# Performance work log

Hardware: AMD Instinct MI355X
Metric: run time of the kernel (lower is better)

Reference implementation:

```python
import jax, jax.numpy as jnp
import numpy as np
from jax import lax

B, N, C, HEADS, SR = 2, 4096, 256, 8, 2
HW = 64

def setup_inputs() -> dict:
    key = jax.random.key(0)
    ks = jax.random.split(key, 12)
    s = 0.02
    return {
        "x0": jax.random.normal(ks[0], (B, N, C), jnp.float32),
        "x1": jax.random.normal(ks[1], (B, N, C), jnp.float32),
        "Wq": jax.random.normal(ks[2], (C, C), jnp.float32) * s,
        "Wkv": jax.random.normal(ks[3], (2 * C, C), jnp.float32) * s,
        "Wproj": jax.random.normal(ks[4], (C, C), jnp.float32) * s,
        "bproj": jnp.zeros((C,), jnp.float32),
        "Wsr": jax.random.normal(ks[5], (C, C, SR, SR), jnp.float32) * np.sqrt(2.0 / (SR * SR * C)),
        "bsr": jnp.zeros((C,), jnp.float32),
        "ln_w0": jnp.ones((C,), jnp.float32),
        "ln_b0": jnp.zeros((C,), jnp.float32),
        "ln_w1": jnp.ones((C,), jnp.float32),
        "ln_b1": jnp.zeros((C,), jnp.float32),
        "H": HW,
        "W": HW,
    }

def _layernorm(x, w, b, eps=1e-5):
    mu = jnp.mean(x, axis=-1, keepdims=True)
    var = jnp.mean(jnp.square(x - mu), axis=-1, keepdims=True)
    return (x - mu) * lax.rsqrt(var + eps) * w + b

def _attend(x, ln_w, ln_b, Wq, Wkv, Wproj, bproj, Wsr, bsr, H, W):
    b, n, c = x.shape
    h = HEADS
    d = c // h
    scale = d ** -0.5
    # q: (B, h, N, d)
    q = (x @ Wq.T).reshape(b, n, h, d).transpose(0, 2, 1, 3)
    # spatial reduction: conv k=stride=sr on (B,C,H,W)
    xs = x.transpose(0, 2, 1).reshape(b, c, H, W)
    xs = lax.conv_general_dilated(xs, Wsr, (SR, SR), 'VALID',
                                  dimension_numbers=('NCHW', 'OIHW', 'NCHW'))
    xs = xs + bsr[None, :, None, None]
    m = (H // SR) * (W // SR)
    xs = xs.reshape(b, c, m).transpose(0, 2, 1)  # (B, M, C)
    xs = _layernorm(xs, ln_w, ln_b)
    kv = (xs @ Wkv.T).reshape(b, m, 2, h, d).transpose(2, 0, 3, 1, 4)
    k, v = kv[0], kv[1]  # (B, h, M, d)
    attn = jnp.einsum('bhnd,bhmd->bhnm', q, k) * scale
    attn = jax.nn.softmax(attn, axis=-1)
    out = jnp.einsum('bhnm,bhmd->bhnd', attn, v)
    out = out.transpose(0, 2, 1, 3).reshape(b, n, c)
    return out @ Wproj.T + bproj

def reference(x0, x1, Wq, Wkv, Wproj, bproj, Wsr, bsr, ln_w0, ln_b0, ln_w1, ln_b1, H, W):
    y0 = _attend(x0, ln_w0, ln_b0, Wq, Wkv, Wproj, bproj, Wsr, bsr, H, W)
    y1 = _attend(x1, ln_w1, ln_b1, Wq, Wkv, Wproj, bproj, Wsr, bsr, H, W)
    return (y0, y1)
```

## Files before the change

kernel.cpp:

```cpp
#include <hip/hip_runtime.h>
#include <hip/hip_bf16.h>
#include <cstddef>

typedef __hip_bfloat16 bf16;
typedef __attribute__((ext_vector_type(8))) short bf16x8;
typedef __attribute__((ext_vector_type(4))) float f32x4;
typedef __attribute__((ext_vector_type(4))) short short4v;

__device__ __forceinline__ float b2f(bf16 v) { return __bfloat162float(v); }
__device__ __forceinline__ bf16 f2b(float v) { return __float2bfloat16(v); }

#define MFMA(a, b, c) __builtin_amdgcn_mfma_f32_16x16x32_bf16((a), (b), (c), 0, 0, 0)

#define WQ_OFF   0
#define WKV_OFF  65536
#define WP_OFF   196608
#define WSR_OFF  262144

__global__ __launch_bounds__(256) void prep_cvt(
    const float* __restrict__ x0, const float* __restrict__ x1,
    bf16* __restrict__ xb,
    const float* __restrict__ Wq, const float* __restrict__ Wkv,
    const float* __restrict__ Wp, const float* __restrict__ Wsr,
    bf16* __restrict__ wb) {
  const int t = threadIdx.x;
  if (blockIdx.x < 1024) {
    const int gid = blockIdx.x * 256 + t;
    for (int i = gid; i < 1048576; i += 262144) {
      const float4 v = (i < 524288) ? ((const float4*)x0)[i]
                                    : ((const float4*)x1)[i - 524288];
      union { bf16 h[4]; short4v s; } u;
      u.h[0] = f2b(v.x); u.h[1] = f2b(v.y); u.h[2] = f2b(v.z); u.h[3] = f2b(v.w);
      ((short4v*)xb)[i] = u.s;
    }
  } else {
    const int gid = (blockIdx.x - 1024) * 256 + t;
    for (int i = gid; i < 524288; i += 131072) {
      float v;
      if (i < WKV_OFF)       v = Wq[i];
      else if (i < WP_OFF)   v = Wkv[i - WKV_OFF];
      else if (i < WSR_OFF)  v = Wp[i - WP_OFF];
      else {
        const int r = i - WSR_OFF;
        const int o = r >> 10, k = r & 1023;
        const int p = k >> 8, c = k & 255;
        v = Wsr[o * 1024 + c * 4 + p];
      }
      wb[i] = f2b(v);
    }
  }
}

#define STAGE_W(W_lds, wgl, ldg)                                             \
  _Pragma("unroll")                                                          \
  for (int u = 0; u < 8; ++u) {                                              \
    const int idx = u * 256 + t;                                             \
    const int wr = idx >> 5;                                                 \
    const int wc = (idx & 31) * 8;                                           \
    *(bf16x8*)&W_lds[wr][wc] = *(const bf16x8*)((wgl) + wr * (ldg) + wc);    \
  }

__global__ __launch_bounds__(256) void qc_mfma(
    const bf16* __restrict__ xb, const bf16* __restrict__ wb,
    const float* __restrict__ bsr, bf16* __restrict__ q,
    bf16* __restrict__ xsb) {
  __shared__ bf16 W_lds[64][264];
  const int t = threadIdx.x;
  const int wave = t >> 6, lane = t & 63, quad = lane >> 4, l16 = lane & 15;
  const int colh = blockIdx.y * 64;

  if (blockIdx.x < 256) {
    const int row0 = blockIdx.x * 64 + wave * 16;
    STAGE_W(W_lds, wb + WQ_OFF + colh * 256, 256);
    __syncthreads();
    const bf16* ap = xb + (row0 + l16) * 256 + quad * 8;
    f32x4 acc[4];
    #pragma unroll
    for (int j = 0; j < 4; ++j) acc[j] = (f32x4){0.f, 0.f, 0.f, 0.f};
    #pragma unroll
    for (int k0 = 0; k0 < 256; k0 += 32) {
      const bf16x8 af = *(const bf16x8*)(ap + k0);
      #pragma unroll
      for (int j = 0; j < 4; ++j) {
        const bf16x8 wf = *(const bf16x8*)&W_lds[j * 16 + l16][k0 + quad * 8];
        acc[j] = MFMA(af, wf, acc[j]);
      }
    }
    const float scale = 0.2550348572f;
    #pragma unroll
    for (int j = 0; j < 4; ++j)
      #pragma unroll
      for (int r = 0; r < 4; ++r)
        q[(row0 + quad * 4 + r) * 256 + colh + j * 16 + l16] =
            f2b(acc[j][r] * scale);
  } else {
    const int bx = blockIdx.x - 256;
    const int row0 = bx * 64 + wave * 16;
    const int mrow = row0 + l16;
    const int ab = mrow >> 10;
    const int m = mrow & 1023;
    const int mi_ = m >> 5, mj = m & 31;
    f32x4 acc[4];
    #pragma unroll
    for (int j = 0; j < 4; ++j) acc[j] = (f32x4){0.f, 0.f, 0.f, 0.f};
    for (int p = 0; p < 4; ++p) {
      __syncthreads();
      STAGE_W(W_lds, wb + WSR_OFF + colh * 1024 + p * 256, 1024);
      __syncthreads();
      const int n = (2 * mi_ + (p >> 1)) * 64 + 2 * mj + (p & 1);
      const bf16* ap = xb + (ab * 4096 + n) * 256 + quad * 8;
      #pragma unroll
      for (int c0 = 0; c0 < 256; c0 += 32) {
        const bf16x8 af = *(const bf16x8*)(ap + c0);
        #pragma unroll
        for (int j = 0; j < 4; ++j) {
          const bf16x8 wf = *(const bf16x8*)&W_lds[j * 16 + l16][c0 + quad * 8];
          acc[j] = MFMA(af, wf, acc[j]);
        }
      }
    }
    #pragma unroll
    for (int j = 0; j < 4; ++j) {
      const int col = colh + j * 16 + l16;
      const float bv = bsr[col];
      #pragma unroll
      for (int r = 0; r < 4; ++r)
        xsb[(row0 + quad * 4 + r) * 256 + col] = f2b(acc[j][r] + bv);
    }
  }
}

__global__ __launch_bounds__(256) void kvln_mfma(
    const bf16* __restrict__ xsb, const bf16* __restrict__ wb,
    const float* __restrict__ w0, const float* __restrict__ b0,
    const float* __restrict__ w1, const float* __restrict__ b1,
    bf16* __restrict__ kbuf, bf16* __restrict__ vbuf_t) {
  __shared__ bf16 W_lds[64][264];
  __shared__ float lnw[256], lnb[256];
  const int t = threadIdx.x;
  const int wave = t >> 6, lane = t & 63, quad = lane >> 4, l16 = lane & 15;
  const int row0 = blockIdx.x * 64 + wave * 16;
  const int colh = blockIdx.y * 64;
  const int a = (blockIdx.x * 64) >> 11;
  lnw[t] = a ? w1[t] : w0[t];
  lnb[t] = a ? b1[t] : b0[t];
  STAGE_W(W_lds, wb + WKV_OFF + colh * 256, 256);
  __syncthreads();

  const bf16* ap = xsb + (row0 + l16) * 256 + quad * 8;
  bf16x8 af[8];
  float sum = 0.f, ss = 0.f;
  #pragma unroll
  for (int i = 0; i < 8; ++i) {
    af[i] = *(const bf16x8*)(ap + i * 32);
    #pragma unroll
    for (int e = 0; e < 8; ++e) {
      const float x = b2f(((bf16*)&af[i])[e]);
      sum += x; ss += x * x;
    }
  }
  sum += __shfl_xor(sum, 16, 64); sum += __shfl_xor(sum, 32, 64);
  ss  += __shfl_xor(ss, 16, 64);  ss  += __shfl_xor(ss, 32, 64);
  const float mu = sum * (1.0f / 256.0f);
  const float var = ss * (1.0f / 256.0f) - mu * mu;
  const float rstd = rsqrtf(var + 1e-5f);
  #pragma unroll
  for (int i = 0; i < 8; ++i) {
    const int cb = i * 32 + quad * 8;
    union { bf16 h[8]; bf16x8 v; } u;
    #pragma unroll
    for (int e = 0; e < 8; ++e) {
      const float x = b2f(((bf16*)&af[i])[e]);
      u.h[e] = f2b((x - mu) * rstd * lnw[cb + e] + lnb[cb + e]);
    }
    af[i] = u.v;
  }

  f32x4 acc[4];
  #pragma unroll
  for (int j = 0; j < 4; ++j) acc[j] = (f32x4){0.f, 0.f, 0.f, 0.f};
  #pragma unroll
  for (int i = 0; i < 8; ++i) {
    #pragma unroll
    for (int j = 0; j < 4; ++j) {
      const bf16x8 wf = *(const bf16x8*)&W_lds[j * 16 + l16][i * 32 + quad * 8];
      acc[j] = MFMA(af[i], wf, acc[j]);
    }
  }
  #pragma unroll
  for (int j = 0; j < 4; ++j) {
    const int o = colh + j * 16 + l16;
    #pragma unroll
    for (int r = 0; r < 4; ++r) {
      const int row = row0 + quad * 4 + r;
      const int m = row & 1023;
      const bf16 val = f2b(acc[j][r]);
      if (o < 256) {
        const int h = o >> 5, d = o & 31;
        kbuf[((row >> 10) * 8 + h) * 32768 + m * 32 + d] = val;
      } else {
        const int o2 = o - 256;
        const int h = o2 >> 5, d = o2 & 31;
        const int rr = m & 63;
        const int mp = (m & ~63) | (rr & 32) | ((rr & 12) << 1) |
                       ((rr & 16) >> 2) | (rr & 3);
        vbuf_t[((row >> 10) * 8 + h) * 32768 + d * 1024 + mp] = val;
      }
    }
  }
}

__global__ __launch_bounds__(256) void attn_mfma(
    const bf16* __restrict__ q, const bf16* __restrict__ kbuf,
    const bf16* __restrict__ vbuf_t, bf16* __restrict__ att) {
  const int abh = blockIdx.y;
  const int ab = abh >> 3;
  const int h = abh & 7;
  const int t = threadIdx.x;
  const int lane = t & 63, quad = lane >> 4, l16 = lane & 15;
  const int qbase = blockIdx.x * 128 + (t >> 6) * 32;

  __shared__ bf16 KT[2][2048];
  __shared__ bf16 VT[2][2048];

  const bf16* kb = kbuf + abh * 32768;
  const bf16* vb = vbuf_t + abh * 32768;

  const int kg = (t >> 6) * 512 + ((t >> 2) & 15) * 32 + (t & 3) * 8;
  const int vg_row = (t >> 7) * 16 + ((t >> 3) & 15);
  const int vg_col = ((t >> 2) & 1) * 32 + (t & 3) * 8;

  bf16x8 qf[2];
  #pragma unroll
  for (int s = 0; s < 2; ++s)
    qf[s] = *(const bf16x8*)(
        q + (ab * 4096 + qbase + s * 16 + l16) * 256 + h * 32 + quad * 8);

  {
    const bf16x8 kr = *(const bf16x8*)(kb + kg);
    const bf16x8 vr = *(const bf16x8*)(vb + vg_row * 1024 + vg_col);
    *(bf16x8*)&KT[0][t * 8] = kr;
    *(bf16x8*)&VT[0][t * 8] = vr;
  }
  __syncthreads();

  f32x4 o[2][2];
  float lp[2] = {0.f, 0.f};
  #pragma unroll
  for (int s = 0; s < 2; ++s) {
    o[s][0] = (f32x4){0.f, 0.f, 0.f, 0.f};
    o[s][1] = (f32x4){0.f, 0.f, 0.f, 0.f};
  }
  const f32x4 zero = {0.f, 0.f, 0.f, 0.f};

  for (int kt = 0; kt < 16; ++kt) {
    const int cur = kt & 1;
    bf16x8 kr, vr;
    const bool pf = (kt + 1 < 16);
    if (pf) {
      const int nk0 = (kt + 1) * 64;
      kr = *(const bf16x8*)(kb + nk0 * 32 + kg);
      vr = *(const bf16x8*)(vb + vg_row * 1024 + nk0 + vg_col);
    }
    f32x4 S[2][4];
    #pragma unroll
    for (int tt = 0; tt < 4; ++tt) {
      const bf16x8 kf =
          *(const bf16x8*)&KT[cur][(tt * 64 + l16 * 4 + quad) * 8];
      S[0][tt] = MFMA(kf, qf[0], zero);
      S[1][tt] = MFMA(kf, qf[1], zero);
    }
    bf16x8 pa[2][2];
    #pragma unroll
    for (int s = 0; s < 2; ++s) {
      float p[4][4];
      float acc = 0.f;
      #pragma unroll
      for (int tt = 0; tt < 4; ++tt)
        #pragma unroll
        for (int r = 0; r < 4; ++r) {
          p[tt][r] = __builtin_amdgcn_exp2f(S[s][tt][r]);
          acc += p[tt][r];
        }
      lp[s] += acc;
      #pragma unroll
      for (int c2 = 0; c2 < 2; ++c2) {
        union { __hip_bfloat162 h2[4]; bf16x8 v; } u;
        u.h2[0] = __float22bfloat162_rn(float2{p[c2 * 2][0], p[c2 * 2][1]});
        u.h2[1] = __float22bfloat162_rn(float2{p[c2 * 2][2], p[c2 * 2][3]});
        u.h2[2] = __float22bfloat162_rn(float2{p[c2 * 2 + 1][0], p[c2 * 2 + 1][1]});
        u.h2[3] = __float22bfloat162_rn(float2{p[c2 * 2 + 1][2], p[c2 * 2 + 1][3]});
        pa[s][c2] = u.v;
      }
    }
    #pragma unroll
    for (int c2 = 0; c2 < 2; ++c2) {
      #pragma unroll
      for (int dh = 0; dh < 2; ++dh) {
        const bf16x8 vf = *(const bf16x8*)&VT[cur]
            [(dh * 128 + l16 * 8 + c2 * 4 + quad) * 8];
        o[0][dh] = MFMA(pa[0][c2], vf, o[0][dh]);
        o[1][dh] = MFMA(pa[1][c2], vf, o[1][dh]);
      }
    }
    if (pf) {
      *(bf16x8*)&KT[cur ^ 1][t * 8] = kr;
      *(bf16x8*)&VT[cur ^ 1][t * 8] = vr;
    }
    __syncthreads();
  }
  #pragma unroll
  for (int s = 0; s < 2; ++s) {
    lp[s] += __shfl_xor(lp[s], 16, 64);
    lp[s] += __shfl_xor(lp[s], 32, 64);
  }
  #pragma unroll
  for (int s = 0; s < 2; ++s) {
    #pragma unroll
    for (int r = 0; r < 4; ++r) {
      const float li = __shfl(lp[s], quad * 4 + r, 16);
      const float inv = 1.0f / li;
      const int qrow = ab * 4096 + qbase + s * 16 + quad * 4 + r;
      bf16* orow = att + qrow * 256 + h * 32;
      orow[l16]      = f2b(o[s][0][r] * inv);
      orow[16 + l16] = f2b(o[s][1][r] * inv);
    }
  }
}

__global__ __launch_bounds__(256) void proj_mfma(
    const bf16* __restrict__ att, const bf16* __restrict__ wb,
    const float* __restrict__ bp, float* __restrict__ outp) {
  __shared__ bf16 W_lds[64][264];
  const int t = threadIdx.x;
  const int wave = t >> 6, lane = t & 63, quad = lane >> 4, l16 = lane & 15;
  const int row0 = blockIdx.x * 64 + wave * 16;
  const int colh = blockIdx.y * 64;
  STAGE_W(W_lds, wb + WP_OFF + colh * 256, 256);
  __syncthreads();
  const bf16* ap = att + (row0 + l16) * 256 + quad * 8;
  f32x4 acc[4];
  #pragma unroll
  for (int j = 0; j < 4; ++j) acc[j] = (f32x4){0.f, 0.f, 0.f, 0.f};
  #pragma unroll
  for (int k0 = 0; k0 < 256; k0 += 32) {
    const bf16x8 af = *(const bf16x8*)(ap + k0);
    #pragma unroll
    for (int j = 0; j < 4; ++j) {
      const bf16x8 wf = *(const bf16x8*)&W_lds[j * 16 + l16][k0 + quad * 8];
      acc[j] = MFMA(af, wf, acc[j]);
    }
  }
  #pragma unroll
  for (int j = 0; j < 4; ++j) {
    const int col = colh + j * 16 + l16;
    const float bv = bp[col];
    #pragma unroll
    for (int r = 0; r < 4; ++r)
      outp[(row0 + quad * 4 + r) * 256 + col] = acc[j][r] + bv;
  }
}

extern "C" void kernel_launch(void* const* d_in, const int* in_sizes, int n_in,
                              void* d_out, int out_size, void* d_ws, size_t ws_size,
                              hipStream_t stream) {
  const float* x0    = (const float*)d_in[0];
  const float* x1    = (const float*)d_in[1];
  const float* Wq    = (const float*)d_in[2];
  const float* Wkv   = (const float*)d_in[3];
  const float* Wproj = (const float*)d_in[4];
  const float* bproj = (const float*)d_in[5];
  const float* Wsr   = (const float*)d_in[6];
  const float* bsr   = (const float*)d_in[7];
  const float* lnw0  = (const float*)d_in[8];
  const float* lnb0  = (const float*)d_in[9];
  const float* lnw1  = (const float*)d_in[10];
  const float* lnb1  = (const float*)d_in[11];

  bf16* q_bf   = (bf16*)d_out;
  bf16* xb     = q_bf + 4194304;
  bf16* att_bf = (bf16*)d_ws;
  bf16* xsb    = att_bf + 4194304;
  bf16* kbuf   = xsb + 1048576;
  bf16* vbuf_t = kbuf + 1048576;
  bf16* wb     = vbuf_t + 1048576;
  float* y     = (float*)d_out;

  const dim3 blk(256);
  prep_cvt<<<dim3(1536), blk, 0, stream>>>(x0, x1, xb, Wq, Wkv, Wproj, Wsr, wb);
  qc_mfma<<<dim3(320, 4), blk, 0, stream>>>(xb, wb, bsr, q_bf, xsb);
  kvln_mfma<<<dim3(64, 8), blk, 0, stream>>>(xsb, wb, lnw0, lnb0, lnw1, lnb1,
                                             kbuf, vbuf_t);
  attn_mfma<<<dim3(32, 32), blk, 0, stream>>>(q_bf, kbuf, vbuf_t, att_bf);
  proj_mfma<<<dim3(256, 4), blk, 0, stream>>>(att_bf, wb, bproj, y);
}
```

Baseline: 158.8 us.

## Fuse all stages into one cooperative persistent kernel with grid syncs

Replaces the five separate launches (convert, q/conv, kv+layernorm, attention, projection) with a single cooperative kernel of 512 persistent blocks that loop over work units and separate stages with grid-wide syncs. The aim is to remove per-launch overhead and inter-kernel gaps. The cost is that each stage now runs on a fixed 512-block grid with grid barriers and threadfences, which can reduce parallelism in some stages. The original multi-kernel path stays as a fallback if the cooperative launch fails.

```diff
diff --git a/kernel.cpp b/kernel.cpp
--- a/kernel.cpp
+++ b/kernel.cpp
@@ -1,6 +1,9 @@
 #include <hip/hip_runtime.h>
 #include <hip/hip_bf16.h>
+#include <hip/hip_cooperative_groups.h>
 #include <cstddef>
+
+namespace cg = cooperative_groups;
 
 typedef __hip_bfloat16 bf16;
 typedef __attribute__((ext_vector_type(8))) short bf16x8;
@@ -16,6 +19,16 @@
 #define WKV_OFF  65536
 #define WP_OFF   196608
 #define WSR_OFF  262144
+
+#define STAGE_W(W_lds, wgl, ldg)                                             \
+  _Pragma("unroll")                                                          \
+  for (int uu_ = 0; uu_ < 8; ++uu_) {                                        \
+    const int idx_ = uu_ * 256 + t;                                          \
+    const int wr_ = idx_ >> 5;                                               \
+    const int wc_ = (idx_ & 31) * 8;                                         \
+    *(bf16x8*)&W_lds[wr_][wc_] = *(const bf16x8*)((wgl) + wr_ * (ldg) + wc_);\
+  }
+
 
 __global__ __launch_bounds__(256) void prep_cvt(
     const float* __restrict__ x0, const float* __restrict__ x1,
@@ -50,15 +63,6 @@
     }
   }
 }
-
-#define STAGE_W(W_lds, wgl, ldg)                                             \
-  _Pragma("unroll")                                                          \
-  for (int u = 0; u < 8; ++u) {                                              \
-    const int idx = u * 256 + t;                                             \
-    const int wr = idx >> 5;                                                 \
-    const int wc = (idx & 31) * 8;                                           \
-    *(bf16x8*)&W_lds[wr][wc] = *(const bf16x8*)((wgl) + wr * (ldg) + wc);    \
-  }
 
 __global__ __launch_bounds__(256) void qc_mfma(
     const bf16* __restrict__ xb, const bf16* __restrict__ wb,
@@ -361,6 +365,342 @@
   }
 }
 
+__global__ __launch_bounds__(256, 2) void mega(
+    const float* x0, const float* x1,
+    const float* Wq, const float* Wkv,
+    const float* Wp, const float* Wsr,
+    const float* bsr, const float* bp,
+    const float* w0, const float* b0,
+    const float* w1, const float* b1,
+    bf16* xb, bf16* wb, bf16* q, bf16* xsb,
+    bf16* kbuf, bf16* vbuf_t, bf16* att, float* y) {
+  cg::grid_group grid = cg::this_grid();
+  __shared__ bf16 W_lds[64][264];
+  __shared__ bf16 KT[2][2048];
+  __shared__ bf16 VT[2][2048];
+  __shared__ float lnw[256], lnb[256];
+
+  const int t = threadIdx.x;
+  const int wave = t >> 6, lane = t & 63, quad = lane >> 4, l16 = lane & 15;
+  const int bid = blockIdx.x;
+  const int NB = gridDim.x;
+
+  {
+    const int gid = bid * 256 + t;
+    const int gs = NB * 256;
+    for (int i = gid; i < 1048576; i += gs) {
+      const float4 v = (i < 524288) ? ((const float4*)x0)[i]
+                                    : ((const float4*)x1)[i - 524288];
+      union { bf16 h[4]; short4v s; } u;
+      u.h[0] = f2b(v.x); u.h[1] = f2b(v.y); u.h[2] = f2b(v.z); u.h[3] = f2b(v.w);
+      ((short4v*)xb)[i] = u.s;
+    }
+    for (int i = gid; i < 524288; i += gs) {
+      float v;
+      if (i < WKV_OFF)       v = Wq[i];
+      else if (i < WP_OFF)   v = Wkv[i - WKV_OFF];
+      else if (i < WSR_OFF)  v = Wp[i - WP_OFF];
+      else {
+        const int r = i - WSR_OFF;
+        const int o = r >> 10, k = r & 1023;
+        const int p = k >> 8, c = k & 255;
+        v = Wsr[o * 1024 + c * 4 + p];
+      }
+      wb[i] = f2b(v);
+    }
+  }
+  __threadfence(); grid.sync(); __threadfence();
+
+  for (int u = bid; u < 512; u += NB) {
+    if (u < 256) {
+      const int cx = u & 63, cy = u >> 6;
+      const int row0 = cx * 64 + wave * 16;
+      const int colh = cy * 64;
+      const int mrow = row0 + l16;
+      const int ab = mrow >> 10;
+      const int m = mrow & 1023;
+      const int mi_ = m >> 5, mj = m & 31;
+      f32x4 acc[4];
+      #pragma unroll
+      for (int j = 0; j < 4; ++j) acc[j] = (f32x4){0.f, 0.f, 0.f, 0.f};
+      for (int p = 0; p < 4; ++p) {
+        __syncthreads();
+        STAGE_W(W_lds, wb + WSR_OFF + colh * 1024 + p * 256, 1024);
+        __syncthreads();
+        const int n = (2 * mi_ + (p >> 1)) * 64 + 2 * mj + (p & 1);
+        const bf16* ap = xb + (ab * 4096 + n) * 256 + quad * 8;
+        #pragma unroll
+        for (int c0 = 0; c0 < 256; c0 += 32) {
+          const bf16x8 af = *(const bf16x8*)(ap + c0);
+          #pragma unroll
+          for (int j = 0; j < 4; ++j) {
+            const bf16x8 wf = *(const bf16x8*)&W_lds[j * 16 + l16][c0 + quad * 8];
+            acc[j] = MFMA(af, wf, acc[j]);
+          }
+        }
+      }
+      #pragma unroll
+      for (int j = 0; j < 4; ++j) {
+        const int col = colh + j * 16 + l16;
+        const float bv = bsr[col];
+        #pragma unroll
+        for (int r = 0; r < 4; ++r)
+          xsb[(row0 + quad * 4 + r) * 256 + col] = f2b(acc[j][r] + bv);
+      }
+    } else {
+      const int idx = u - 256;
+      const int colh = (idx >> 6) * 64;
+      __syncthreads();
+      STAGE_W(W_lds, wb + WQ_OFF + colh * 256, 256);
+      __syncthreads();
+      const float scale = 0.2550348572f;
+      for (int ii = 0; ii < 4; ++ii) {
+        const int row0 = ((idx & 63) * 4 + ii) * 64 + wave * 16;
+        const bf16* ap = xb + (row0 + l16) * 256 + quad * 8;
+        f32x4 acc[4];
+        #pragma unroll
+        for (int j = 0; j < 4; ++j) acc[j] = (f32x4){0.f, 0.f, 0.f, 0.f};
+        #pragma unroll
+        for (int k0 = 0; k0 < 256; k0 += 32) {
+          const bf16x8 af = *(const bf16x8*)(ap + k0);
+          #pragma unroll
+          for (int j = 0; j < 4; ++j) {
+            const bf16x8 wf = *(const bf16x8*)&W_lds[j * 16 + l16][k0 + quad * 8];
+            acc[j] = MFMA(af, wf, acc[j]);
+          }
+        }
+        #pragma unroll
+        for (int j = 0; j < 4; ++j)
+          #pragma unroll
+          for (int r = 0; r < 4; ++r)
+            q[(row0 + quad * 4 + r) * 256 + colh + j * 16 + l16] =
+                f2b(acc[j][r] * scale);
+      }
+    }
+  }
+  __threadfence(); grid.sync(); __threadfence();
+
+  for (int u = bid; u < 512; u += NB) {
+    const int kx = u & 63;
+    const int colh = (u >> 6) * 64;
+    const int row0 = kx * 64 + wave * 16;
+    const int a = (kx * 64) >> 11;
+    __syncthreads();
+    lnw[t] = a ? w1[t] : w0[t];
+    lnb[t] = a ? b1[t] : b0[t];
+    STAGE_W(W_lds, wb + WKV_OFF + colh * 256, 256);
+    __syncthreads();
+
+    const bf16* ap = xsb + (row0 + l16) * 256 + quad * 8;
+    bf16x8 af[8];
+    float sum = 0.f, ss = 0.f;
+    #pragma unroll
+    for (int i = 0; i < 8; ++i) {
+      af[i] = *(const bf16x8*)(ap + i * 32);
+      #pragma unroll
+      for (int e = 0; e < 8; ++e) {
+        const float x = b2f(((bf16*)&af[i])[e]);
+        sum += x; ss += x * x;
+      }
+    }
+    sum += __shfl_xor(sum, 16, 64); sum += __shfl_xor(sum, 32, 64);
+    ss  += __shfl_xor(ss, 16, 64);  ss  += __shfl_xor(ss, 32, 64);
+    const float mu = sum * (1.0f / 256.0f);
+    const float var = ss * (1.0f / 256.0f) - mu * mu;
+    const float rstd = rsqrtf(var + 1e-5f);
+    #pragma unroll
+    for (int i = 0; i < 8; ++i) {
+      const int cb = i * 32 + quad * 8;
+      union { bf16 h[8]; bf16x8 v; } uu;
+      #pragma unroll
+      for (int e = 0; e < 8; ++e) {
+        const float x = b2f(((bf16*)&af[i])[e]);
+        uu.h[e] = f2b((x - mu) * rstd * lnw[cb + e] + lnb[cb + e]);
+      }
+      af[i] = uu.v;
+    }
+
+    f32x4 acc[4];
+    #pragma unroll
+    for (int j = 0; j < 4; ++j) acc[j] = (f32x4){0.f, 0.f, 0.f, 0.f};
+    #pragma unroll
+    for (int i = 0; i < 8; ++i) {
+      #pragma unroll
+      for (int j = 0; j < 4; ++j) {
+        const bf16x8 wf = *(const bf16x8*)&W_lds[j * 16 + l16][i * 32 + quad * 8];
+        acc[j] = MFMA(af[i], wf, acc[j]);
+      }
+    }
+    #pragma unroll
+    for (int j = 0; j < 4; ++j) {
+      const int o = colh + j * 16 + l16;
+      #pragma unroll
+      for (int r = 0; r < 4; ++r) {
+        const int row = row0 + quad * 4 + r;
+        const int m = row & 1023;
+        const bf16 val = f2b(acc[j][r]);
+        if (o < 256) {
+          const int h = o >> 5, d = o & 31;
+          kbuf[((row >> 10) * 8 + h) * 32768 + m * 32 + d] = val;
+        } else {
+          const int o2 = o - 256;
+          const int h = o2 >> 5, d = o2 & 31;
+          const int rr = m & 63;
+          const int mp = (m & ~63) | (rr & 32) | ((rr & 12) << 1) |
+                         ((rr & 16) >> 2) | (rr & 3);
+          vbuf_t[((row >> 10) * 8 + h) * 32768 + d * 1024 + mp] = val;
+        }
+      }
+    }
+  }
+  __threadfence(); grid.sync(); __threadfence();
+
+  {
+    const int kg = (t >> 6) * 512 + ((t >> 2) & 15) * 32 + (t & 3) * 8;
+    const int vg_row = (t >> 7) * 16 + ((t >> 3) & 15);
+    const int vg_col = ((t >> 2) & 1) * 32 + (t & 3) * 8;
+    const f32x4 zero = {0.f, 0.f, 0.f, 0.f};
+
+    for (int unit = bid; unit < 1024; unit += NB) {
+      const int abh = unit >> 5;
+      const int ab = abh >> 3;
+      const int h = abh & 7;
+      const int qbase = (unit & 31) * 128 + wave * 32;
+
+      const bf16* kb = kbuf + abh * 32768;
+      const bf16* vb = vbuf_t + abh * 32768;
+
+      bf16x8 qf[2];
+      #pragma unroll
+      for (int s = 0; s < 2; ++s)
+        qf[s] = *(const bf16x8*)(
+            q + (ab * 4096 + qbase + s * 16 + l16) * 256 + h * 32 + quad * 8);
+
+      {
+        const bf16x8 kr = *(const bf16x8*)(kb + kg);
+        const bf16x8 vr = *(const bf16x8*)(vb + vg_row * 1024 + vg_col);
+        *(bf16x8*)&KT[0][t * 8] = kr;
+        *(bf16x8*)&VT[0][t * 8] = vr;
+      }
+      __syncthreads();
+
+      f32x4 o[2][2];
+      float lp[2] = {0.f, 0.f};
+      #pragma unroll
+      for (int s = 0; s < 2; ++s) {
+        o[s][0] = (f32x4){0.f, 0.f, 0.f, 0.f};
+        o[s][1] = (f32x4){0.f, 0.f, 0.f, 0.f};
+      }
+
+      for (int kt = 0; kt < 16; ++kt) {
+        const int cur = kt & 1;
+        bf16x8 kr, vr;
+        const bool pfl = (kt + 1 < 16);
+        if (pfl) {
+          const int nk0 = (kt + 1) * 64;
+          kr = *(const bf16x8*)(kb + nk0 * 32 + kg);
+          vr = *(const bf16x8*)(vb + vg_row * 1024 + nk0 + vg_col);
+        }
+        f32x4 S[2][4];
+        #pragma unroll
+        for (int tt = 0; tt < 4; ++tt) {
+          const bf16x8 kf =
+              *(const bf16x8*)&KT[cur][(tt * 64 + l16 * 4 + quad) * 8];
+          S[0][tt] = MFMA(kf, qf[0], zero);
+          S[1][tt] = MFMA(kf, qf[1], zero);
+        }
+        bf16x8 pa[2][2];
+        #pragma unroll
+        for (int s = 0; s < 2; ++s) {
+          float p[4][4];
+          float acc = 0.f;
+          #pragma unroll
+          for (int tt = 0; tt < 4; ++tt)
+            #pragma unroll
+            for (int r = 0; r < 4; ++r) {
+              p[tt][r] = __builtin_amdgcn_exp2f(S[s][tt][r]);
+              acc += p[tt][r];
+            }
+          lp[s] += acc;
+          #pragma unroll
+          for (int c2 = 0; c2 < 2; ++c2) {
+            union { __hip_bfloat162 h2[4]; bf16x8 v; } uu;
+            uu.h2[0] = __float22bfloat162_rn(float2{p[c2 * 2][0], p[c2 * 2][1]});
+            uu.h2[1] = __float22bfloat162_rn(float2{p[c2 * 2][2], p[c2 * 2][3]});
+            uu.h2[2] = __float22bfloat162_rn(float2{p[c2 * 2 + 1][0], p[c2 * 2 + 1][1]});
+            uu.h2[3] = __float22bfloat162_rn(float2{p[c2 * 2 + 1][2], p[c2 * 2 + 1][3]});
+            pa[s][c2] = uu.v;
+          }
+        }
+        #pragma unroll
+        for (int c2 = 0; c2 < 2; ++c2) {
+          #pragma unroll
+          for (int dh = 0; dh < 2; ++dh) {
+            const bf16x8 vf = *(const bf16x8*)&VT[cur]
+                [(dh * 128 + l16 * 8 + c2 * 4 + quad) * 8];
+            o[0][dh] = MFMA(pa[0][c2], vf, o[0][dh]);
+            o[1][dh] = MFMA(pa[1][c2], vf, o[1][dh]);
+          }
+        }
+        if (pfl) {
+          *(bf16x8*)&KT[cur ^ 1][t * 8] = kr;
+          *(bf16x8*)&VT[cur ^ 1][t * 8] = vr;
+        }
+        __syncthreads();
+      }
+      #pragma unroll
+      for (int s = 0; s < 2; ++s) {
+        lp[s] += __shfl_xor(lp[s], 16, 64);
+        lp[s] += __shfl_xor(lp[s], 32, 64);
+      }
+      #pragma unroll
+      for (int s = 0; s < 2; ++s) {
+        #pragma unroll
+        for (int r = 0; r < 4; ++r) {
+          const float li = __shfl(lp[s], quad * 4 + r, 16);
+          const float inv = 1.0f / li;
+          const int qrow = ab * 4096 + qbase + s * 16 + quad * 4 + r;
+          bf16* orow = att + qrow * 256 + h * 32;
+          orow[l16]      = f2b(o[s][0][r] * inv);
+          orow[16 + l16] = f2b(o[s][1][r] * inv);
+        }
+      }
+    }
+  }
+  __threadfence(); grid.sync(); __threadfence();
+
+  for (int u = bid; u < 512; u += NB) {
+    const int colh = (u >> 7) * 64;
+    __syncthreads();
+    STAGE_W(W_lds, wb + WP_OFF + colh * 256, 256);
+    __syncthreads();
+    for (int ii = 0; ii < 2; ++ii) {
+      const int row0 = ((u & 127) * 2 + ii) * 64 + wave * 16;
+      const bf16* ap = att + (row0 + l16) * 256 + quad * 8;
+      f32x4 acc[4];
+      #pragma unroll
+      for (int j = 0; j < 4; ++j) acc[j] = (f32x4){0.f, 0.f, 0.f, 0.f};
+      #pragma unroll
+      for (int k0 = 0; k0 < 256; k0 += 32) {
+        const bf16x8 af = *(const bf16x8*)(ap + k0);
+        #pragma unroll
+        for (int j = 0; j < 4; ++j) {
+          const bf16x8 wf = *(const bf16x8*)&W_lds[j * 16 + l16][k0 + quad * 8];
+          acc[j] = MFMA(af, wf, acc[j]);
+        }
+      }
+      #pragma unroll
+      for (int j = 0; j < 4; ++j) {
+        const int col = colh + j * 16 + l16;
+        const float bv = bp[col];
+        #pragma unroll
+        for (int r = 0; r < 4; ++r)
+          y[(row0 + quad * 4 + r) * 256 + col] = acc[j][r] + bv;
+      }
+    }
+  }
+}
+
 extern "C" void kernel_launch(void* const* d_in, const int* in_sizes, int n_in,
                               void* d_out, int out_size, void* d_ws, size_t ws_size,
                               hipStream_t stream) {
@@ -386,11 +726,37 @@
   bf16* wb     = vbuf_t + 1048576;
   float* y     = (float*)d_out;
 
-  const dim3 blk(256);
-  prep_cvt<<<dim3(1536), blk, 0, stream>>>(x0, x1, xb, Wq, Wkv, Wproj, Wsr, wb);
-  qc_mfma<<<dim3(320, 4), blk, 0, stream>>>(xb, wb, bsr, q_bf, xsb);
-  kvln_mfma<<<dim3(64, 8), blk, 0, stream>>>(xsb, wb, lnw0, lnb0, lnw1, lnb1,
-                                             kbuf, vbuf_t);
-  attn_mfma<<<dim3(32, 32), blk, 0, stream>>>(q_bf, kbuf, vbuf_t, att_bf);
-  proj_mfma<<<dim3(256, 4), blk, 0, stream>>>(att_bf, wb, bproj, y);
+  static int coop_ok = -1;
+  if (coop_ok < 0) {
+    int maxB = 0;
+    hipError_t e =
+        hipOccupancyMaxActiveBlocksPerMultiprocessor(&maxB, mega, 256, 0);
+    coop_ok = (e == hipSuccess && maxB >= 2) ? 1 : 0;
+  }
+
+  bool launched = false;
+  if (coop_ok == 1) {
+    void* args[] = {
+        (void*)&x0, (void*)&x1, (void*)&Wq, (void*)&Wkv, (void*)&Wproj,
+        (void*)&Wsr, (void*)&bsr, (void*)&bproj, (void*)&lnw0, (void*)&lnb0,
+        (void*)&lnw1, (void*)&lnb1, (void*)&xb, (void*)&wb, (void*)&q_bf,
+        (void*)&xsb, (void*)&kbuf, (void*)&vbuf_t, (void*)&att_bf, (void*)&y};
+    hipError_t e = hipLaunchCooperativeKernel(mega, dim3(512), dim3(256),
+                                              args, 0u, stream);
+    if (e == hipSuccess) {
+      launched = true;
+    } else {
+      coop_ok = 0;
+    }
+  }
+
+  if (!launched) {
+    const dim3 blk(256);
+    prep_cvt<<<dim3(1536), blk, 0, stream>>>(x0, x1, xb, Wq, Wkv, Wproj, Wsr, wb);
+    qc_mfma<<<dim3(320, 4), blk, 0, stream>>>(xb, wb, bsr, q_bf, xsb);
+    kvln_mfma<<<dim3(64, 8), blk, 0, stream>>>(xsb, wb, lnw0, lnb0, lnw1, lnb1,
+                                               kbuf, vbuf_t);
+    attn_mfma<<<dim3(32, 32), blk, 0, stream>>>(q_bf, kbuf, vbuf_t, att_bf);
+    proj_mfma<<<dim3(256, 4), blk, 0, stream>>>(att_bf, wb, bproj, y);
+  }
 }
```

Measured after the change: 160.7 us. No clear change (+1.2%).

## Fuse fp32-to-bf16 conversion into GEMM kernels and swizzle V tile in LDS

Applied to the files above, without the earlier changes.

Removes the separate prep_cvt kernel and converts x and all weight matrices from fp32 to bf16 on the fly inside the Q/conv, KV and projection kernels. This saves one launch and a full round trip of the converted activations through global memory. The cost is that each GEMM now reads fp32 data, twice the bytes per element, and x is re-read by each of the 4 column blocks. The conv weight gather is also strided. Separately, the V tile in LDS is XOR-swizzled on write and read to reduce bank conflicts in the attention PV MFMA loads.

```diff
diff --git a/kernel.cpp b/kernel.cpp
--- a/kernel.cpp
+++ b/kernel.cpp
@@ -12,56 +12,49 @@
 
 #define MFMA(a, b, c) __builtin_amdgcn_mfma_f32_16x16x32_bf16((a), (b), (c), 0, 0, 0)
 
-#define WQ_OFF   0
-#define WKV_OFF  65536
-#define WP_OFF   196608
-#define WSR_OFF  262144
-
-__global__ __launch_bounds__(256) void prep_cvt(
+__device__ __forceinline__ bf16x8 cvt8f(const float* p) {
+  const float4 a = *(const float4*)p;
+  const float4 b = *(const float4*)(p + 4);
+  union { __hip_bfloat162 h2[4]; bf16x8 v; } u;
+  u.h2[0] = __float22bfloat162_rn(float2{a.x, a.y});
+  u.h2[1] = __float22bfloat162_rn(float2{a.z, a.w});
+  u.h2[2] = __float22bfloat162_rn(float2{b.x, b.y});
+  u.h2[3] = __float22bfloat162_rn(float2{b.z, b.w});
+  return u.v;
+}
+
+__device__ __forceinline__ const float* xrow_ptr(
+    const float* x0, const float* x1, int rr) {
+  return (rr < 8192) ? (x0 + rr * 256) : (x1 + (rr - 8192) * 256);
+}
+
+#define STAGE_WF(W_lds, wgl, ldg)                                            \
+  _Pragma("unroll")                                                          \
+  for (int uu_ = 0; uu_ < 8; ++uu_) {                                        \
+    const int idx_ = uu_ * 256 + t;                                          \
+    const int wr_ = idx_ >> 5;                                               \
+    const int wc_ = (idx_ & 31) * 8;                                         \
+    *(bf16x8*)&W_lds[wr_][wc_] = cvt8f((wgl) + wr_ * (ldg) + wc_);           \
+  }
+
+#define STAGE_WSR(W_lds, Wsr, colh, p)                                       \
+  _Pragma("unroll")                                                          \
+  for (int uu_ = 0; uu_ < 8; ++uu_) {                                        \
+    const int idx_ = uu_ * 256 + t;                                          \
+    const int wr_ = idx_ >> 5;                                               \
+    const int wc_ = (idx_ & 31) * 8;                                         \
+    const float* wp_ = (Wsr) + ((colh) + wr_) * 1024 + wc_ * 4 + (p);        \
+    union { __hip_bfloat162 h2[4]; bf16x8 v; } u_;                           \
+    u_.h2[0] = __float22bfloat162_rn(float2{wp_[0],  wp_[4]});               \
+    u_.h2[1] = __float22bfloat162_rn(float2{wp_[8],  wp_[12]});              \
+    u_.h2[2] = __float22bfloat162_rn(float2{wp_[16], wp_[20]});              \
+    u_.h2[3] = __float22bfloat162_rn(float2{wp_[24], wp_[28]});              \
+    *(bf16x8*)&W_lds[wr_][wc_] = u_.v;                                       \
+  }
+
+__global__ __launch_bounds__(256) void qc_mfma(
     const float* __restrict__ x0, const float* __restrict__ x1,
-    bf16* __restrict__ xb,
-    const float* __restrict__ Wq, const float* __restrict__ Wkv,
-    const float* __restrict__ Wp, const float* __restrict__ Wsr,
-    bf16* __restrict__ wb) {
-  const int t = threadIdx.x;
-  if (blockIdx.x < 1024) {
-    const int gid = blockIdx.x * 256 + t;
-    for (int i = gid; i < 1048576; i += 262144) {
-      const float4 v = (i < 524288) ? ((const float4*)x0)[i]
-                                    : ((const float4*)x1)[i - 524288];
-      union { bf16 h[4]; short4v s; } u;
-      u.h[0] = f2b(v.x); u.h[1] = f2b(v.y); u.h[2] = f2b(v.z); u.h[3] = f2b(v.w);
-      ((short4v*)xb)[i] = u.s;
-    }
-  } else {
-    const int gid = (blockIdx.x - 1024) * 256 + t;
-    for (int i = gid; i < 524288; i += 131072) {
-      float v;
-      if (i < WKV_OFF)       v = Wq[i];
-      else if (i < WP_OFF)   v = Wkv[i - WKV_OFF];
-      else if (i < WSR_OFF)  v = Wp[i - WP_OFF];
-      else {
-        const int r = i - WSR_OFF;
-        const int o = r >> 10, k = r & 1023;
-        const int p = k >> 8, c = k & 255;
-        v = Wsr[o * 1024 + c * 4 + p];
-      }
-      wb[i] = f2b(v);
-    }
-  }
-}
-
-#define STAGE_W(W_lds, wgl, ldg)                                             \
-  _Pragma("unroll")                                                          \
-  for (int u = 0; u < 8; ++u) {                                              \
-    const int idx = u * 256 + t;                                             \
-    const int wr = idx >> 5;                                                 \
-    const int wc = (idx & 31) * 8;                                           \
-    *(bf16x8*)&W_lds[wr][wc] = *(const bf16x8*)((wgl) + wr * (ldg) + wc);    \
-  }
-
-__global__ __launch_bounds__(256) void qc_mfma(
-    const bf16* __restrict__ xb, const bf16* __restrict__ wb,
+    const float* __restrict__ Wq, const float* __restrict__ Wsr,
     const float* __restrict__ bsr, bf16* __restrict__ q,
     bf16* __restrict__ xsb) {
   __shared__ bf16 W_lds[64][264];
@@ -71,15 +64,15 @@
 
   if (blockIdx.x < 256) {
     const int row0 = blockIdx.x * 64 + wave * 16;
-    STAGE_W(W_lds, wb + WQ_OFF + colh * 256, 256);
+    STAGE_WF(W_lds, Wq + colh * 256, 256);
     __syncthreads();
-    const bf16* ap = xb + (row0 + l16) * 256 + quad * 8;
+    const float* ap = xrow_ptr(x0, x1, row0 + l16) + quad * 8;
     f32x4 acc[4];
     #pragma unroll
     for (int j = 0; j < 4; ++j) acc[j] = (f32x4){0.f, 0.f, 0.f, 0.f};
     #pragma unroll
     for (int k0 = 0; k0 < 256; k0 += 32) {
-      const bf16x8 af = *(const bf16x8*)(ap + k0);
+      const bf16x8 af = cvt8f(ap + k0);
       #pragma unroll
       for (int j = 0; j < 4; ++j) {
         const bf16x8 wf = *(const bf16x8*)&W_lds[j * 16 + l16][k0 + quad * 8];
@@ -105,13 +98,13 @@
     for (int j = 0; j < 4; ++j) acc[j] = (f32x4){0.f, 0.f, 0.f, 0.f};
     for (int p = 0; p < 4; ++p) {
       __syncthreads();
-      STAGE_W(W_lds, wb + WSR_OFF + colh * 1024 + p * 256, 1024);
+      STAGE_WSR(W_lds, Wsr, colh, p);
       __syncthreads();
       const int n = (2 * mi_ + (p >> 1)) * 64 + 2 * mj + (p & 1);
-      const bf16* ap = xb + (ab * 4096 + n) * 256 + quad * 8;
+      const float* ap = xrow_ptr(x0, x1, ab * 4096 + n) + quad * 8;
       #pragma unroll
       for (int c0 = 0; c0 < 256; c0 += 32) {
-        const bf16x8 af = *(const bf16x8*)(ap + c0);
+        const bf16x8 af = cvt8f(ap + c0);
         #pragma unroll
         for (int j = 0; j < 4; ++j) {
           const bf16x8 wf = *(const bf16x8*)&W_lds[j * 16 + l16][c0 + quad * 8];
@@ -131,7 +124,7 @@
 }
 
 __global__ __launch_bounds__(256) void kvln_mfma(
-    const bf16* __restrict__ xsb, const bf16* __restrict__ wb,
+    const bf16* __restrict__ xsb, const float* __restrict__ Wkv,
     const float* __restrict__ w0, const float* __restrict__ b0,
     const float* __restrict__ w1, const float* __restrict__ b1,
     bf16* __restrict__ kbuf, bf16* __restrict__ vbuf_t) {
@@ -144,7 +137,7 @@
   const int a = (blockIdx.x * 64) >> 11;
   lnw[t] = a ? w1[t] : w0[t];
   lnb[t] = a ? b1[t] : b0[t];
-  STAGE_W(W_lds, wb + WKV_OFF + colh * 256, 256);
+  STAGE_WF(W_lds, Wkv + colh * 256, 256);
   __syncthreads();
 
   const bf16* ap = xsb + (row0 + l16) * 256 + quad * 8;
@@ -229,6 +222,7 @@
   const int kg = (t >> 6) * 512 + ((t >> 2) & 15) * 32 + (t & 3) * 8;
   const int vg_row = (t >> 7) * 16 + ((t >> 3) & 15);
   const int vg_col = ((t >> 2) & 1) * 32 + (t & 3) * 8;
+  const int vt_w = (t ^ ((t >> 3) & 7)) * 8;
 
   bf16x8 qf[2];
   #pragma unroll
@@ -240,7 +234,7 @@
     const bf16x8 kr = *(const bf16x8*)(kb + kg);
     const bf16x8 vr = *(const bf16x8*)(vb + vg_row * 1024 + vg_col);
     *(bf16x8*)&KT[0][t * 8] = kr;
-    *(bf16x8*)&VT[0][t * 8] = vr;
+    *(bf16x8*)&VT[0][vt_w] = vr;
   }
   __syncthreads();
 
@@ -297,15 +291,16 @@
     for (int c2 = 0; c2 < 2; ++c2) {
       #pragma unroll
       for (int dh = 0; dh < 2; ++dh) {
-        const bf16x8 vf = *(const bf16x8*)&VT[cur]
-            [(dh * 128 + l16 * 8 + c2 * 4 + quad) * 8];
+        const int vti =
+            ((dh * 128 + l16 * 8 + c2 * 4 + quad) ^ (l16 & 7)) * 8;
+        const bf16x8 vf = *(const bf16x8*)&VT[cur][vti];
         o[0][dh] = MFMA(pa[0][c2], vf, o[0][dh]);
         o[1][dh] = MFMA(pa[1][c2], vf, o[1][dh]);
       }
     }
     if (pf) {
       *(bf16x8*)&KT[cur ^ 1][t * 8] = kr;
-      *(bf16x8*)&VT[cur ^ 1][t * 8] = vr;
+      *(bf16x8*)&VT[cur ^ 1][vt_w] = vr;
     }
     __syncthreads();
   }
@@ -329,14 +324,14 @@
 }
 
 __global__ __launch_bounds__(256) void proj_mfma(
-    const bf16* __restrict__ att, const bf16* __restrict__ wb,
+    const bf16* __restrict__ att, const float* __restrict__ Wp,
     const float* __restrict__ bp, float* __restrict__ outp) {
   __shared__ bf16 W_lds[64][264];
   const int t = threadIdx.x;
   const int wave = t >> 6, lane = t & 63, quad = lane >> 4, l16 = lane & 15;
   const int row0 = blockIdx.x * 64 + wave * 16;
   const int colh = blockIdx.y * 64;
-  STAGE_W(W_lds, wb + WP_OFF + colh * 256, 256);
+  STAGE_WF(W_lds, Wp + colh * 256, 256);
   __syncthreads();
   const bf16* ap = att + (row0 + l16) * 256 + quad * 8;
   f32x4 acc[4];
@@ -378,19 +373,16 @@
   const float* lnb1  = (const float*)d_in[11];
 
   bf16* q_bf   = (bf16*)d_out;
-  bf16* xb     = q_bf + 4194304;
   bf16* att_bf = (bf16*)d_ws;
   bf16* xsb    = att_bf + 4194304;
   bf16* kbuf   = xsb + 1048576;
   bf16* vbuf_t = kbuf + 1048576;
-  bf16* wb     = vbuf_t + 1048576;
   float* y     = (float*)d_out;
 
   const dim3 blk(256);
-  prep_cvt<<<dim3(1536), blk, 0, stream>>>(x0, x1, xb, Wq, Wkv, Wproj, Wsr, wb);
-  qc_mfma<<<dim3(320, 4), blk, 0, stream>>>(xb, wb, bsr, q_bf, xsb);
-  kvln_mfma<<<dim3(64, 8), blk, 0, stream>>>(xsb, wb, lnw0, lnb0, lnw1, lnb1,
+  qc_mfma<<<dim3(320, 4), blk, 0, stream>>>(x0, x1, Wq, Wsr, bsr, q_bf, xsb);
+  kvln_mfma<<<dim3(64, 8), blk, 0, stream>>>(xsb, Wkv, lnw0, lnb0, lnw1, lnb1,
                                              kbuf, vbuf_t);
   attn_mfma<<<dim3(32, 32), blk, 0, stream>>>(q_bf, kbuf, vbuf_t, att_bf);
-  proj_mfma<<<dim3(256, 4), blk, 0, stream>>>(att_bf, wb, bproj, y);
-}
+  proj_mfma<<<dim3(256, 4), blk, 0, stream>>>(att_bf, Wproj, bproj, y);
+}
```

Result: slower. 216.5 us (+36.3%).
